# Optimization experiments

Measured on AMD Instinct MI355X. Metric: run time of the kernel, lower is better.

Reference implementation:

```python
import jax, jax.numpy as jnp
import numpy as np

C = 36   # num_classes
H = 256  # hidden_dim


def setup_inputs() -> dict:
    key = jax.random.key(0)
    ks = jax.random.split(key, 12)
    B, L, Dl, Dg = 32, 196, 1024, 1024
    s = lambda d: 1.0 / np.sqrt(d)
    return {
        "local_features": jax.random.normal(ks[0], (B, L, Dl), jnp.float32),
        "global_average_pool": jax.random.normal(ks[1], (B, Dg), jnp.float32),
        "Wl": jax.random.normal(ks[2], (Dl, C * H), jnp.float32) * s(Dl),
        "bl": jax.random.normal(ks[3], (C * H,), jnp.float32) * s(Dl),
        "Wg": jax.random.normal(ks[4], (Dg, C * H), jnp.float32) * s(Dg),
        "bg": jax.random.normal(ks[5], (C * H,), jnp.float32) * s(Dg),
        "Wh": jax.random.normal(ks[6], (H, H), jnp.float32) * s(H),
        "bh": jax.random.normal(ks[7], (H,), jnp.float32) * s(H),
        "Wr": jax.random.normal(ks[8], (H, 4), jnp.float32) * s(H),
        "br": jax.random.normal(ks[9], (4,), jnp.float32) * s(H),
        "Wc": jax.random.normal(ks[10], (H, 1), jnp.float32) * s(H),
        "bc": jax.random.normal(ks[11], (1,), jnp.float32) * s(H),
    }


def reference(local_features, global_average_pool, Wl, bl, Wg, bg, Wh, bh, Wr, br, Wc, bc):
    B, L, _ = local_features.shape
    # global projection -> [B, C, H]
    xg = (global_average_pool @ Wg + bg).reshape(B, C, H)
    # local projection -> [B, L, C, H] -> [B, C, L, H]
    xl = (local_features @ Wl + bl).reshape(B, L, C, H).transpose(0, 2, 1, 3)
    # per-class attention scores over locations: [B, C, L]
    dot = jnp.einsum('bch,bclh->bcl', xg, xl)
    attn = jax.nn.softmax(dot, axis=-1)
    # attention-weighted sum over locations: [B, C, H]
    ws = jnp.einsum('bcl,bclh->bch', attn, xl)
    hid = jax.nn.relu(ws @ Wh + bh)
    bbox_coords = (hid @ Wr + br).reshape(B, C * 4)   # [B, 4C]
    bbox_presence = (hid @ Wc + bc)[..., 0]           # [B, C]
    return bbox_coords, bbox_presence
```

## Files before the change

### kernel.cpp

```cpp
#include <hip/hip_runtime.h>
#include <hip/hip_bf16.h>
#include <stdint.h>

#define NCLS 36
#define HDIM 256
#define BSZ  32
#define LLOC 196
#define DIN  1024
#define NCH  9216
#define XG_N 294912
#define SC_N 225792
#define V_N  1179648

__global__ __launch_bounds__(256) void kA_xg_part(
    const float* __restrict__ Wg, const float* __restrict__ gap,
    float* __restrict__ A) {
  __shared__ __align__(16) float4 gs[512];
  const int tid = threadIdx.x;
  const int nt = blockIdx.x, ks = blockIdx.y, bh = blockIdx.z;
  const int kc = ks * 128, b0 = bh * 16;
  for (int i = tid; i < 512; i += 256) {
    int bi = i >> 5, pos = i & 31;
    gs[bi * 32 + pos] = *(const float4*)&gap[(size_t)(b0 + bi) * DIN + kc + pos * 4];
  }
  __syncthreads();
  const int g = tid >> 7, lane = tid & 127;
  const int n = nt * 256 + lane;
  float acc0[8] = {0,0,0,0,0,0,0,0};
  float acc1[8] = {0,0,0,0,0,0,0,0};
  const float* wp = Wg + (size_t)kc * NCH + n;
  for (int k4 = 0; k4 < 32; ++k4) {
    float w10 = wp[(size_t)(k4 * 4 + 0) * NCH];
    float w11 = wp[(size_t)(k4 * 4 + 1) * NCH];
    float w12 = wp[(size_t)(k4 * 4 + 2) * NCH];
    float w13 = wp[(size_t)(k4 * 4 + 3) * NCH];
    float w20 = wp[(size_t)(k4 * 4 + 0) * NCH + 128];
    float w21 = wp[(size_t)(k4 * 4 + 1) * NCH + 128];
    float w22 = wp[(size_t)(k4 * 4 + 2) * NCH + 128];
    float w23 = wp[(size_t)(k4 * 4 + 3) * NCH + 128];
    #pragma unroll
    for (int bi = 0; bi < 8; ++bi) {
      float4 gv = gs[(g * 8 + bi) * 32 + k4];
      acc0[bi] += gv.x * w10 + gv.y * w11 + gv.z * w12 + gv.w * w13;
      acc1[bi] += gv.x * w20 + gv.y * w21 + gv.z * w22 + gv.w * w23;
    }
  }
  #pragma unroll
  for (int bi = 0; bi < 8; ++bi) {
    size_t o = (size_t)ks * XG_N + (size_t)(b0 + g * 8 + bi) * NCH + n;
    A[o]       = acc0[bi];
    A[o + 128] = acc1[bi];
  }
}

__global__ __launch_bounds__(256) void kC_V(
    const float* __restrict__ Wl, const float* __restrict__ A,
    const float* __restrict__ bg, float* __restrict__ V) {
  __shared__ __align__(16) float4 xs[512];
  const int tid = threadIdx.x;
  const int c = blockIdx.x, kq = blockIdx.y, b0 = blockIdx.z * 8;
  for (int i = tid; i < 512; i += 256) {
    int bi = i >> 6, j = i & 63;
    size_t off = (size_t)(b0 + bi) * NCH + c * HDIM + j * 4;
    float4 s = *(const float4*)&bg[c * HDIM + j * 4];
    #pragma unroll
    for (int p = 0; p < 8; ++p) {
      float4 t = *(const float4*)&A[(size_t)p * XG_N + off];
      s.x += t.x; s.y += t.y; s.z += t.z; s.w += t.w;
    }
    xs[bi * 64 + j] = s;
  }
  __syncthreads();
  const int g = tid >> 7, lane = tid & 127;
  const int k1 = kq * 256 + lane, k2 = k1 + 128;
  float acc0[4] = {0,0,0,0};
  float acc1[4] = {0,0,0,0};
  const float* wl1 = Wl + (size_t)k1 * NCH + c * HDIM;
  const float* wl2 = Wl + (size_t)k2 * NCH + c * HDIM;
  for (int j = 0; j < 64; ++j) {
    float4 w1 = *(const float4*)&wl1[j * 4];
    float4 w2 = *(const float4*)&wl2[j * 4];
    #pragma unroll
    for (int bi = 0; bi < 4; ++bi) {
      float4 x = xs[(g * 4 + bi) * 64 + j];
      acc0[bi] += w1.x * x.x + w1.y * x.y + w1.z * x.z + w1.w * x.w;
      acc1[bi] += w2.x * x.x + w2.y * x.y + w2.z * x.z + w2.w * x.w;
    }
  }
  #pragma unroll
  for (int bi = 0; bi < 4; ++bi) {
    size_t o = (size_t)((b0 + g * 4 + bi) * NCLS + c) * DIN;
    V[o + k1] = acc0[bi];
    V[o + k2] = acc1[bi];
  }
}

__global__ __launch_bounds__(256) void kD_scores(
    const float* __restrict__ local_f, const float* __restrict__ V,
    float* __restrict__ A) {
  __shared__ __align__(16) float4 vs[384];
  const int tid = threadIdx.x;
  const int b = blockIdx.x, cg = blockIdx.y, ks = blockIdx.z;
  for (int i = tid; i < 384; i += 256) {
    int ci = i >> 5, pos = i & 31;
    vs[ci * 32 + pos] = *(const float4*)&V[(size_t)(b * NCLS + cg * 12 + ci) * DIN
                                           + ks * 128 + pos * 4];
  }
  __syncthreads();
  const int g = tid >> 7, p = tid & 127;
  if (p >= 98) return;
  const int l1 = p, l2 = p + 98;
  const float* lp1 = local_f + (size_t)(b * LLOC + l1) * DIN + ks * 128;
  const float* lp2 = local_f + (size_t)(b * LLOC + l2) * DIN + ks * 128;
  float acc0[6] = {0,0,0,0,0,0};
  float acc1[6] = {0,0,0,0,0,0};
  for (int j = 0; j < 32; ++j) {
    float4 a1 = *(const float4*)&lp1[j * 4];
    float4 a2 = *(const float4*)&lp2[j * 4];
    #pragma unroll
    for (int ci = 0; ci < 6; ++ci) {
      float4 v = vs[(g * 6 + ci) * 32 + j];
      acc0[ci] += a1.x * v.x + a1.y * v.y + a1.z * v.z + a1.w * v.w;
      acc1[ci] += a2.x * v.x + a2.y * v.y + a2.z * v.z + a2.w * v.w;
    }
  }
  #pragma unroll
  for (int ci = 0; ci < 6; ++ci) {
    size_t o = (size_t)ks * SC_N + (size_t)(b * NCLS + cg * 12 + g * 6 + ci) * LLOC;
    A[o + l1] = acc0[ci];
    A[o + l2] = acc1[ci];
  }
}

__global__ __launch_bounds__(64) void kE_softmax(
    const float* __restrict__ A, float* __restrict__ attn2) {
  const int b = blockIdx.x, c = blockIdx.y, t = threadIdx.x;
  const size_t base = (size_t)(b * NCLS + c) * LLOC;
  float sc[4];
  int nl = 0;
  float m = -1e30f;
  for (int l = t; l < LLOC; l += 64) {
    float s = 0.f;
    #pragma unroll
    for (int p = 0; p < 8; ++p) s += A[(size_t)p * SC_N + base + l];
    sc[nl++] = s; m = fmaxf(m, s);
  }
  #pragma unroll
  for (int off = 32; off >= 1; off >>= 1) m = fmaxf(m, __shfl_xor(m, off));
  float sum = 0.f;
  for (int i = 0; i < nl; ++i) { sc[i] = __expf(sc[i] - m); sum += sc[i]; }
  #pragma unroll
  for (int off = 32; off >= 1; off >>= 1) sum += __shfl_xor(sum, off);
  float inv = 1.0f / sum;
  nl = 0;
  for (int l = t; l < LLOC; l += 64) attn2[base + l] = sc[nl++] * inv;
}

__global__ __launch_bounds__(256) void kF_U(
    const float* __restrict__ local_f, const float* __restrict__ attn2,
    float* __restrict__ U) {
  __shared__ __align__(16) float4 as4[588];
  const int tid = threadIdx.x;
  const int b = blockIdx.x, ksf = blockIdx.y, cgf = blockIdx.z;
  for (int i = tid; i < 588; i += 256) {
    int ci = i / 49, pos = i - ci * 49;
    as4[ci * 49 + pos] = *(const float4*)&attn2[(size_t)(b * NCLS + cgf * 12 + ci) * LLOC
                                                + pos * 4];
  }
  __syncthreads();
  const int q = tid >> 6, lane = tid & 63;
  const int k1 = ksf * 128 + lane, k2 = k1 + 64;
  const int cb = q * 3;
  float acc0[3] = {0,0,0};
  float acc1[3] = {0,0,0};
  const float* lp1 = local_f + (size_t)b * LLOC * DIN + k1;
  const float* lp2 = lp1 + 64;
  for (int l4 = 0; l4 < 49; ++l4) {
    float a10 = lp1[(size_t)(l4 * 4 + 0) * DIN];
    float a11 = lp1[(size_t)(l4 * 4 + 1) * DIN];
    float a12 = lp1[(size_t)(l4 * 4 + 2) * DIN];
    float a13 = lp1[(size_t)(l4 * 4 + 3) * DIN];
    float a20 = lp2[(size_t)(l4 * 4 + 0) * DIN];
    float a21 = lp2[(size_t)(l4 * 4 + 1) * DIN];
    float a22 = lp2[(size_t)(l4 * 4 + 2) * DIN];
    float a23 = lp2[(size_t)(l4 * 4 + 3) * DIN];
    #pragma unroll
    for (int ci = 0; ci < 3; ++ci) {
      float4 w = as4[(cb + ci) * 49 + l4];
      acc0[ci] += a10 * w.x + a11 * w.y + a12 * w.z + a13 * w.w;
      acc1[ci] += a20 * w.x + a21 * w.y + a22 * w.z + a23 * w.w;
    }
  }
  #pragma unroll
  for (int ci = 0; ci < 3; ++ci) {
    size_t o = (size_t)(b * NCLS + cgf * 12 + cb + ci) * DIN;
    U[o + k1] = acc0[ci];
    U[o + k2] = acc1[ci];
  }
}

__global__ __launch_bounds__(256) void kG_ws(
    const float* __restrict__ Wl, const float* __restrict__ U,
    float* __restrict__ A) {
  __shared__ __align__(16) float4 us[512];
  const int tid = threadIdx.x;
  const int c = blockIdx.x, ksg = blockIdx.y, b0 = blockIdx.z * 16;
  const int kc = ksg * 128;
  for (int i = tid; i < 512; i += 256) {
    int bi = i >> 5, pos = i & 31;
    us[bi * 32 + pos] = *(const float4*)&U[(size_t)((b0 + bi) * NCLS + c) * DIN
                                           + kc + pos * 4];
  }
  __syncthreads();
  const int g = tid >> 7, lane = tid & 127;
  float acc0[8] = {0,0,0,0,0,0,0,0};
  float acc1[8] = {0,0,0,0,0,0,0,0};
  const float* wp = Wl + (size_t)kc * NCH + c * HDIM + lane;
  for (int k4 = 0; k4 < 32; ++k4) {
    float w10 = wp[(size_t)(k4 * 4 + 0) * NCH];
    float w11 = wp[(size_t)(k4 * 4 + 1) * NCH];
    float w12 = wp[(size_t)(k4 * 4 + 2) * NCH];
    float w13 = wp[(size_t)(k4 * 4 + 3) * NCH];
    float w20 = wp[(size_t)(k4 * 4 + 0) * NCH + 128];
    float w21 = wp[(size_t)(k4 * 4 + 1) * NCH + 128];
    float w22 = wp[(size_t)(k4 * 4 + 2) * NCH + 128];
    float w23 = wp[(size_t)(k4 * 4 + 3) * NCH + 128];
    #pragma unroll
    for (int bi = 0; bi < 8; ++bi) {
      float4 u = us[(g * 8 + bi) * 32 + k4];
      acc0[bi] += u.x * w10 + u.y * w11 + u.z * w12 + u.w * w13;
      acc1[bi] += u.x * w20 + u.y * w21 + u.z * w22 + u.w * w23;
    }
  }
  #pragma unroll
  for (int bi = 0; bi < 8; ++bi) {
    size_t o = (size_t)ksg * XG_N + (size_t)(b0 + g * 8 + bi) * NCH + c * HDIM + lane;
    A[o]       = acc0[bi];
    A[o + 128] = acc1[bi];
  }
}

__global__ __launch_bounds__(256) void kH_heads(
    const float* __restrict__ Wh, const float* __restrict__ bh,
    const float* __restrict__ Wr, const float* __restrict__ br,
    const float* __restrict__ Wc, const float* __restrict__ bc,
    const float* __restrict__ bl,
    const float* __restrict__ A, float* __restrict__ out) {
  __shared__ float ws_s[3][HDIM];
  __shared__ float hid_s[3][HDIM];
  const int b = blockIdx.x, c0 = blockIdx.y * 3;
  const int j = threadIdx.x;
  #pragma unroll
  for (int ci = 0; ci < 3; ++ci) {
    size_t base = (size_t)b * NCH + (c0 + ci) * HDIM + j;
    float s = bl[(c0 + ci) * HDIM + j];
    #pragma unroll
    for (int p = 0; p < 8; ++p) s += A[(size_t)p * XG_N + base];
    ws_s[ci][j] = s;
  }
  __syncthreads();
  float acc[3] = {0,0,0};
  for (int h = 0; h < HDIM; ++h) {
    float whj = Wh[(size_t)h * HDIM + j];
    acc[0] += ws_s[0][h] * whj;
    acc[1] += ws_s[1][h] * whj;
    acc[2] += ws_s[2][h] * whj;
  }
  float bj = bh[j];
  #pragma unroll
  for (int ci = 0; ci < 3; ++ci) hid_s[ci][j] = fmaxf(acc[ci] + bj, 0.0f);
  __syncthreads();
  const int r = j >> 6, j0 = j & 63;
  for (int ci = 0; ci < 3; ++ci) {
    const int c = c0 + ci;
    float s = 0.f;
    #pragma unroll
    for (int m = 0; m < 4; ++m)
      s += hid_s[ci][j0 + 64 * m] * Wr[(j0 + 64 * m) * 4 + r];
    #pragma unroll
    for (int off = 32; off >= 1; off >>= 1) s += __shfl_xor(s, off);
    if (j0 == 0) out[(size_t)b * (NCLS * 4) + c * 4 + r] = s + br[r];
    if (r == 0) {
      float p = 0.f;
      #pragma unroll
      for (int m = 0; m < 4; ++m)
        p += hid_s[ci][j0 + 64 * m] * Wc[j0 + 64 * m];
      #pragma unroll
      for (int off = 32; off >= 1; off >>= 1) p += __shfl_xor(p, off);
      if (j0 == 0) out[BSZ * NCLS * 4 + b * NCLS + c] = p + bc[0];
    }
  }
}

extern "C" void kernel_launch(void* const* d_in, const int* in_sizes, int n_in,
                              void* d_out, int out_size, void* d_ws, size_t ws_size,
                              hipStream_t stream) {
  const float* local = (const float*)d_in[0];
  const float* gap   = (const float*)d_in[1];
  const float* Wl    = (const float*)d_in[2];
  const float* bl    = (const float*)d_in[3];
  const float* Wg    = (const float*)d_in[4];
  const float* bg    = (const float*)d_in[5];
  const float* Wh    = (const float*)d_in[6];
  const float* bh    = (const float*)d_in[7];
  const float* Wr    = (const float*)d_in[8];
  const float* br    = (const float*)d_in[9];
  const float* Wc    = (const float*)d_in[10];
  const float* bc    = (const float*)d_in[11];
  float* out         = (float*)d_out;

  float* A     = (float*)d_ws;
  float* V     = A + (size_t)8 * XG_N;
  float* attn2 = V + V_N;
  float* U     = attn2 + SC_N;

  kA_xg_part<<<dim3(36, 8, 2), dim3(256), 0, stream>>>(Wg, gap, A);
  kC_V      <<<dim3(36, 4, 4), dim3(256), 0, stream>>>(Wl, A, bg, V);
  kD_scores <<<dim3(32, 3, 8), dim3(256), 0, stream>>>(local, V, A);
  kE_softmax<<<dim3(32, 36),   dim3(64),  0, stream>>>(A, attn2);
  kF_U      <<<dim3(32, 8, 3), dim3(256), 0, stream>>>(local, attn2, U);
  kG_ws     <<<dim3(36, 8, 2), dim3(256), 0, stream>>>(Wl, U, A);
  kH_heads  <<<dim3(32, 12),   dim3(256), 0, stream>>>(Wh, bh, Wr, br, Wc, bc, bl, A, out);
}
```

Baseline: 296.3 us.

## Retile kC_V for coalesced Wl reads and more batch reuse per block

Rewrites the V = Wl·xg kernel so that four lanes share one Wl row and read contiguous float4s. This coalesces the Wl loads, which were previously strided by a full row per lane. Each block now handles 16 batches instead of 8, and each thread keeps 32 accumulators, so every Wl load is reused more. A quad shuffle reduction then combines the partial sums. The cost is higher register pressure, fewer active lanes when writing results, and a changed grid shape.

```diff
diff --git a/kernel.cpp b/kernel.cpp
--- a/kernel.cpp
+++ b/kernel.cpp
@@ -56,42 +56,60 @@
 __global__ __launch_bounds__(256) void kC_V(
     const float* __restrict__ Wl, const float* __restrict__ A,
     const float* __restrict__ bg, float* __restrict__ V) {
-  __shared__ __align__(16) float4 xs[512];
-  const int tid = threadIdx.x;
-  const int c = blockIdx.x, kq = blockIdx.y, b0 = blockIdx.z * 8;
-  for (int i = tid; i < 512; i += 256) {
-    int bi = i >> 6, j = i & 63;
-    size_t off = (size_t)(b0 + bi) * NCH + c * HDIM + j * 4;
-    float4 s = *(const float4*)&bg[c * HDIM + j * 4];
+  __shared__ __align__(16) float4 xg_s[1024];
+  const int tid = threadIdx.x;
+  const int c  = blockIdx.x;
+  const int kt = blockIdx.y;
+  const int b0 = blockIdx.z * 16;
+
+  const float4* bg4 = (const float4*)bg;
+  for (int i = tid; i < 1024; i += 256) {
+    int bi = i >> 6, hq = i & 63;
+    float4 s = bg4[c * 64 + hq];
+    size_t off4 = ((size_t)(b0 + bi) * NCH >> 2) + c * 64 + hq;
     #pragma unroll
     for (int p = 0; p < 8; ++p) {
-      float4 t = *(const float4*)&A[(size_t)p * XG_N + off];
+      float4 t = *((const float4*)A + (size_t)p * (XG_N / 4) + off4);
       s.x += t.x; s.y += t.y; s.z += t.z; s.w += t.w;
     }
-    xs[bi * 64 + j] = s;
-  }
-  __syncthreads();
-  const int g = tid >> 7, lane = tid & 127;
-  const int k1 = kq * 256 + lane, k2 = k1 + 128;
-  float acc0[4] = {0,0,0,0};
-  float acc1[4] = {0,0,0,0};
-  const float* wl1 = Wl + (size_t)k1 * NCH + c * HDIM;
-  const float* wl2 = Wl + (size_t)k2 * NCH + c * HDIM;
-  for (int j = 0; j < 64; ++j) {
-    float4 w1 = *(const float4*)&wl1[j * 4];
-    float4 w2 = *(const float4*)&wl2[j * 4];
-    #pragma unroll
-    for (int bi = 0; bi < 4; ++bi) {
-      float4 x = xs[(g * 4 + bi) * 64 + j];
+    xg_s[bi * 64 + hq] = s;
+  }
+  __syncthreads();
+
+  const int w    = tid >> 6;
+  const int lane = tid & 63;
+  const int q    = lane & 3;
+  const int r    = lane >> 2;
+  const int k1   = kt * 128 + w * 32 + r;
+  const int k2   = k1 + 16;
+
+  float acc0[16] = {0,0,0,0,0,0,0,0,0,0,0,0,0,0,0,0};
+  float acc1[16] = {0,0,0,0,0,0,0,0,0,0,0,0,0,0,0,0};
+  const float* wl1 = Wl + (size_t)k1 * NCH + c * HDIM + q * 4;
+  const float* wl2 = Wl + (size_t)k2 * NCH + c * HDIM + q * 4;
+  #pragma unroll 4
+  for (int it = 0; it < 16; ++it) {
+    float4 w1 = *(const float4*)(wl1 + it * 16);
+    float4 w2 = *(const float4*)(wl2 + it * 16);
+    #pragma unroll
+    for (int bi = 0; bi < 16; ++bi) {
+      float4 x = xg_s[bi * 64 + it * 4 + q];
       acc0[bi] += w1.x * x.x + w1.y * x.y + w1.z * x.z + w1.w * x.w;
       acc1[bi] += w2.x * x.x + w2.y * x.y + w2.z * x.z + w2.w * x.w;
     }
   }
   #pragma unroll
-  for (int bi = 0; bi < 4; ++bi) {
-    size_t o = (size_t)((b0 + g * 4 + bi) * NCLS + c) * DIN;
-    V[o + k1] = acc0[bi];
-    V[o + k2] = acc1[bi];
+  for (int bi = 0; bi < 16; ++bi) {
+    acc0[bi] += __shfl_xor(acc0[bi], 1); acc0[bi] += __shfl_xor(acc0[bi], 2);
+    acc1[bi] += __shfl_xor(acc1[bi], 1); acc1[bi] += __shfl_xor(acc1[bi], 2);
+  }
+  if (q == 0) {
+    #pragma unroll
+    for (int bi = 0; bi < 16; ++bi) {
+      size_t o = (size_t)((b0 + bi) * NCLS + c) * DIN;
+      V[o + k1] = acc0[bi];
+      V[o + k2] = acc1[bi];
+    }
   }
 }
 
@@ -315,7 +333,7 @@
   float* U     = attn2 + SC_N;
 
   kA_xg_part<<<dim3(36, 8, 2), dim3(256), 0, stream>>>(Wg, gap, A);
-  kC_V      <<<dim3(36, 4, 4), dim3(256), 0, stream>>>(Wl, A, bg, V);
+  kC_V      <<<dim3(36, 8, 2), dim3(256), 0, stream>>>(Wl, A, bg, V);
   kD_scores <<<dim3(32, 3, 8), dim3(256), 0, stream>>>(local, V, A);
   kE_softmax<<<dim3(32, 36),   dim3(64),  0, stream>>>(A, attn2);
   kF_U      <<<dim3(32, 8, 3), dim3(256), 0, stream>>>(local, attn2, U);
```

Measured after the change: 267.2 us. -9.8%, faster.
